# Kernel optimization log

Hardware: AMD Instinct MI355X
Metric: run time of the kernel (lower is better)

## Reference

```python
import jax, jax.numpy as jnp
import numpy as np

N = 8192
IN_DIM = 256
OUT_DIM = 64
ALPHA = 0.2  # LeakyReLU negative slope


def setup_inputs() -> dict:
    key = jax.random.key(0)
    k1, k2, k3 = jax.random.split(key, 3)
    h = jax.random.normal(k1, (N, IN_DIM), dtype=jnp.float32)
    adj = jnp.zeros((N, N), dtype=jnp.bool_)  # accepted by forward but unused (faithful to source)
    # xavier_uniform-ish scale for params
    W = jax.random.normal(k2, (IN_DIM, OUT_DIM), dtype=jnp.float32) * (1.414 * (2.0 / (IN_DIM + OUT_DIM)) ** 0.5)
    a = jax.random.normal(k3, (2 * OUT_DIM, 1), dtype=jnp.float32) * (1.414 * (2.0 / (2 * OUT_DIM + 1)) ** 0.5)
    return {"h": h, "adj": adj, "W": W, "a": a}


def reference(h, adj, W, a):
    # Wh: [N, D]
    Wh = h @ W
    d = Wh.shape[1]
    Wh1 = Wh @ a[:d]   # [N, 1]
    Wh2 = Wh @ a[d:]   # [N, 1]
    # e: [N, N] dense additive attention scores (adj is NOT used in the source)
    e = jax.nn.leaky_relu(Wh1 + Wh2.T, negative_slope=ALPHA)
    attention = jax.nn.softmax(e, axis=1)
    # dropout(p=0.6) is identity in eval mode
    h_prime = attention @ Wh  # [N, D]
    return jax.nn.elu(h_prime)
```

## Files before the change

kernel.cpp:

```cpp
#include <hip/hip_runtime.h>
#include <math.h>

#define NN 8192
#define KDIM 256
#define DD 64
#define NB 4096
#define NBLK 256
#define NTHR 512
#define RPB 32
#define CH 32
#define NCH 256
#define LRALPHA 0.2f

__device__ __forceinline__ unsigned f2k(float f) {
    unsigned u = __float_as_uint(f);
    return u ^ ((u >> 31) ? 0xFFFFFFFFu : 0x80000000u);
}
__device__ __forceinline__ float k2f(unsigned k) {
    return __uint_as_float((k & 0x80000000u) ? (k ^ 0x80000000u) : ~k);
}
__device__ __forceinline__ unsigned bucket_of(unsigned key, unsigned kmin, float scale) {
    unsigned d = key - kmin;
    unsigned b = (unsigned)((float)d * scale);
    return b > (NB - 1) ? (NB - 1) : b;
}

__device__ __forceinline__ void  cstf(float* p, float v) { __hip_atomic_store(p, v, __ATOMIC_RELAXED, __HIP_MEMORY_SCOPE_AGENT); }
__device__ __forceinline__ float cldf(const float* p)    { return __hip_atomic_load((float*)p, __ATOMIC_RELAXED, __HIP_MEMORY_SCOPE_AGENT); }
__device__ __forceinline__ unsigned cldu(const unsigned* p) { return __hip_atomic_load((unsigned*)p, __ATOMIC_RELAXED, __HIP_MEMORY_SCOPE_AGENT); }
__device__ __forceinline__ void cstu(unsigned* p, unsigned v) { __hip_atomic_store(p, v, __ATOMIC_RELAXED, __HIP_MEMORY_SCOPE_AGENT); }

__device__ __forceinline__ void gridbar(unsigned* flags, unsigned* rel, unsigned phase) {
    asm volatile("s_waitcnt vmcnt(0)" ::: "memory");
    __syncthreads();
    const int t = threadIdx.x;
    if (blockIdx.x == 0) {
        if (t == 0)
            cstu(&flags[0], phase);
        if (t < NBLK) {
            while (cldu(&flags[t]) < phase)
                __builtin_amdgcn_s_sleep(1);
        }
        __syncthreads();
        if (t == 0)
            cstu(rel, phase);
    } else {
        if (t == 0) {
            cstu(&flags[blockIdx.x], phase);
            while (cldu(rel) < phase)
                __builtin_amdgcn_s_sleep(1);
        }
        __syncthreads();
    }
}

__global__ __launch_bounds__(NTHR, 2) void k_fused(
    const float* __restrict__ h, const float* __restrict__ W,
    const float* __restrict__ a, float* __restrict__ out,
    float* Wh2g, float* sv, float* wnv, float* wpv, float* sg,
    float* cs_neg, float* cs_pos, float* cs_sn, float* cs_sp,
    float* PN, float* SP, float* PNs, float* SPs,
    int* cnt, unsigned* flags, unsigned* rel, unsigned* done)
{
    __shared__ int      ls_bstart[NB + 1];
    __shared__ float    ls_wh1[RPB];
    __shared__ float    ls_wh2[RPB];
    __shared__ unsigned ls_ra[8], ls_rb[8];
    __shared__ int      ls_wsum[8];
    __shared__ float    ls_cs[8][2 * DD];
    __shared__ float    ls_css[16];
    __shared__ float    ls_M2, ls_scale;
    __shared__ unsigned ls_kmin;

    const int t = threadIdx.x, bid = blockIdx.x;
    const int wv = t >> 6, lane = t & 63;
    const int rowBase = bid * RPB;

    float myrow[4];
    {
        const int r0 = rowBase + wv * 4;
        float acc0 = 0.f, acc1 = 0.f, acc2 = 0.f, acc3 = 0.f;
        #pragma unroll 2
        for (int k4 = 0; k4 < KDIM / 4; ++k4) {
            float w0 = W[(4 * k4 + 0) * DD + lane];
            float w1 = W[(4 * k4 + 1) * DD + lane];
            float w2 = W[(4 * k4 + 2) * DD + lane];
            float w3 = W[(4 * k4 + 3) * DD + lane];
            float4 h0 = *(const float4*)(h + (size_t)(r0 + 0) * KDIM + 4 * k4);
            float4 h1 = *(const float4*)(h + (size_t)(r0 + 1) * KDIM + 4 * k4);
            float4 h2 = *(const float4*)(h + (size_t)(r0 + 2) * KDIM + 4 * k4);
            float4 h3 = *(const float4*)(h + (size_t)(r0 + 3) * KDIM + 4 * k4);
            acc0 = fmaf(h0.x, w0, acc0); acc0 = fmaf(h0.y, w1, acc0);
            acc0 = fmaf(h0.z, w2, acc0); acc0 = fmaf(h0.w, w3, acc0);
            acc1 = fmaf(h1.x, w0, acc1); acc1 = fmaf(h1.y, w1, acc1);
            acc1 = fmaf(h1.z, w2, acc1); acc1 = fmaf(h1.w, w3, acc1);
            acc2 = fmaf(h2.x, w0, acc2); acc2 = fmaf(h2.y, w1, acc2);
            acc2 = fmaf(h2.z, w2, acc2); acc2 = fmaf(h2.w, w3, acc2);
            acc3 = fmaf(h3.x, w0, acc3); acc3 = fmaf(h3.y, w1, acc3);
            acc3 = fmaf(h3.z, w2, acc3); acc3 = fmaf(h3.w, w3, acc3);
        }
        myrow[0] = acc0; myrow[1] = acc1; myrow[2] = acc2; myrow[3] = acc3;
        float a1 = a[lane], a2 = a[DD + lane];
        #pragma unroll
        for (int i = 0; i < 4; ++i) {
            float r1 = myrow[i] * a1, r2 = myrow[i] * a2;
            #pragma unroll
            for (int off = 32; off > 0; off >>= 1) {
                r1 += __shfl_xor(r1, off, 64);
                r2 += __shfl_xor(r2, off, 64);
            }
            if (lane == 0) {
                cstf(&Wh2g[r0 + i], r2);
                ls_wh1[wv * 4 + i] = r1;
                ls_wh2[wv * 4 + i] = r2;
            }
        }
    }
    gridbar(flags, rel, 1);

    for (int i = t; i < NB; i += NTHR) ls_bstart[i] = 0;
    float v16[16];
    #pragma unroll
    for (int q = 0; q < 16; ++q)
        v16[q] = cldf(&Wh2g[t + q * NTHR]);
    {
        unsigned lmin = 0xFFFFFFFFu, lmax = 0u;
        #pragma unroll
        for (int q = 0; q < 16; ++q) {
            unsigned k = f2k(v16[q]);
            lmin = min(lmin, k); lmax = max(lmax, k);
        }
        #pragma unroll
        for (int off = 32; off > 0; off >>= 1) {
            lmin = min(lmin, (unsigned)__shfl_xor((int)lmin, off, 64));
            lmax = max(lmax, (unsigned)__shfl_xor((int)lmax, off, 64));
        }
        if (lane == 0) { ls_ra[wv] = lmin; ls_rb[wv] = lmax; }
    }
    __syncthreads();
    if (t == 0) {
        unsigned mn = ls_ra[0], mx = ls_rb[0];
        for (int i = 1; i < 8; ++i) { mn = min(mn, ls_ra[i]); mx = max(mx, ls_rb[i]); }
        ls_kmin = mn;
        ls_scale = (float)NB / ((float)(mx - mn) + 1.0f);
        ls_M2 = k2f(mx);
    }
    __syncthreads();
    const unsigned kmin = ls_kmin;
    const float scale = ls_scale;
    const float M2 = ls_M2;

    #pragma unroll
    for (int q = 0; q < 16; ++q)
        atomicAdd(&ls_bstart[bucket_of(f2k(v16[q]), kmin, scale)], 1);
    __syncthreads();
    {
        int s[8]; int tot = 0;
        #pragma unroll
        for (int j = 0; j < 8; ++j) { s[j] = ls_bstart[8 * t + j]; tot += s[j]; }
        int x = tot;
        #pragma unroll
        for (int off = 1; off < 64; off <<= 1) {
            int y = __shfl_up(x, off, 64);
            if (lane >= off) x += y;
        }
        if (lane == 63) ls_wsum[wv] = x;
        __syncthreads();
        int woff = 0;
        for (int w2 = 0; w2 < wv; ++w2) woff += ls_wsum[w2];
        int acc = woff + x - tot;
        #pragma unroll
        for (int j = 0; j < 8; ++j) { ls_bstart[8 * t + j] = acc; acc += s[j]; }
        if (t == 0) ls_bstart[NB] = NN;
    }
    __syncthreads();
    {
        int posl = 0;
        if (lane < 4) {
            unsigned b = bucket_of(f2k(ls_wh2[wv * 4 + lane]), kmin, scale);
            posl = ls_bstart[b] + atomicAdd(&cnt[b], 1);
        }
        #pragma unroll
        for (int i = 0; i < 4; ++i) {
            int lr = wv * 4 + i;
            float x = ls_wh2[lr];
            int pos = __shfl(posl, i, 64);
            cstf(&sg[(size_t)pos * DD + lane], myrow[i]);
            if (lane == 0) {
                cstf(&sv[pos], x);
                cstf(&wnv[pos], expf(LRALPHA * (x - M2)));
                cstf(&wpv[pos], expf(x - M2));
            }
        }
    }
    gridbar(flags, rel, 2);

    {
        int base = bid * CH + wv * 4;
        float g4[4], wn4[4], wp4[4];
        #pragma unroll
        for (int kk = 0; kk < 4; ++kk) {
            int k = base + kk;
            g4[kk]  = cldf(&sg[(size_t)k * DD + lane]);
            wn4[kk] = cldf(&wnv[k]);
            wp4[kk] = cldf(&wpv[k]);
        }
        float an = 0.f, ap = 0.f, sn = 0.f, sp = 0.f;
        #pragma unroll
        for (int kk = 0; kk < 4; ++kk) {
            an = fmaf(wn4[kk], g4[kk], an); ap = fmaf(wp4[kk], g4[kk], ap);
            sn += wn4[kk]; sp += wp4[kk];
        }
        ls_cs[wv][lane] = an; ls_cs[wv][DD + lane] = ap;
        if (lane == 0) { ls_css[wv] = sn; ls_css[8 + wv] = sp; }
        __syncthreads();
        if (wv == 0) {
            float s = 0.f;
            #pragma unroll
            for (int w2 = 0; w2 < 8; ++w2) s += ls_cs[w2][lane];
            cstf(&cs_neg[bid * DD + lane], s);
            if (lane == 0) { float ss = 0.f; for (int w2 = 0; w2 < 8; ++w2) ss += ls_css[w2]; cstf(&cs_sn[bid], ss); }
        } else if (wv == 1) {
            float s = 0.f;
            #pragma unroll
            for (int w2 = 0; w2 < 8; ++w2) s += ls_cs[w2][DD + lane];
            cstf(&cs_pos[bid * DD + lane], s);
            if (lane == 0) { float ss = 0.f; for (int w2 = 0; w2 < 8; ++w2) ss += ls_css[8 + w2]; cstf(&cs_sp[bid], ss); }
        }
    }
    asm volatile("s_waitcnt vmcnt(0)" ::: "memory");
    __syncthreads();
    if (t == 0)
        cstu(&flags[bid], 3u);

    if (bid == 0) {
        if (t < NBLK) { while (cldu(&flags[t]) < 3u) __builtin_amdgcn_s_sleep(1); }
        __syncthreads();
        const int c0 = wv * 32;
        float v[32];
        #pragma unroll
        for (int j = 0; j < 32; ++j) v[j] = cldf(&cs_neg[(c0 + j) * DD + lane]);
        float tot = 0.f;
        #pragma unroll
        for (int j = 0; j < 32; ++j) tot += v[j];
        ls_cs[wv][lane] = tot;
        __syncthreads();
        float acc = 0.f;
        for (int w2 = 0; w2 < wv; ++w2) acc += ls_cs[w2][lane];
        #pragma unroll
        for (int j = 0; j < 32; ++j) { cstf(&PN[(c0 + j) * DD + lane], acc); acc += v[j]; }
        if (wv == 7) cstf(&PN[NCH * DD + lane], acc);
        asm volatile("s_waitcnt vmcnt(0)" ::: "memory");
        __syncthreads();
        if (t == 0) cstu(&done[0], 1u);
    } else if (bid == 1) {
        if (t < NBLK) { while (cldu(&flags[t]) < 3u) __builtin_amdgcn_s_sleep(1); }
        __syncthreads();
        const int c0 = wv * 32;
        float v[32];
        #pragma unroll
        for (int j = 0; j < 32; ++j) v[j] = cldf(&cs_pos[(c0 + j) * DD + lane]);
        float tot = 0.f;
        #pragma unroll
        for (int j = 0; j < 32; ++j) tot += v[j];
        ls_cs[wv][lane] = tot;
        __syncthreads();
        float acc = 0.f;
        for (int w2 = wv + 1; w2 < 8; ++w2) acc += ls_cs[w2][lane];
        #pragma unroll
        for (int j = 31; j >= 0; --j) { acc += v[j]; cstf(&SP[(c0 + j) * DD + lane], acc); }
        if (wv == 7) cstf(&SP[NCH * DD + lane], 0.f);
        asm volatile("s_waitcnt vmcnt(0)" ::: "memory");
        __syncthreads();
        if (t == 0) cstu(&done[1], 1u);
    } else if (bid == 2) {
        if (t < NBLK) { while (cldu(&flags[t]) < 3u) __builtin_amdgcn_s_sleep(1); }
        __syncthreads();
        if (wv == 0) {
            float s[4];
            #pragma unroll
            for (int j = 0; j < 4; ++j) s[j] = cldf(&cs_sn[4 * lane + j]);
            float tot = s[0] + s[1] + s[2] + s[3];
            float x = tot;
            #pragma unroll
            for (int off = 1; off < 64; off <<= 1) {
                float y = __shfl_up(x, off, 64);
                if (lane >= off) x += y;
            }
            float acc = x - tot;
            #pragma unroll
            for (int j = 0; j < 4; ++j) { cstf(&PNs[4 * lane + j], acc); acc += s[j]; }
            if (lane == 63) cstf(&PNs[NCH], acc);
        } else if (wv == 1) {
            float s[4];
            #pragma unroll
            for (int j = 0; j < 4; ++j) s[j] = cldf(&cs_sp[4 * lane + j]);
            float tot = s[0] + s[1] + s[2] + s[3];
            float x = tot;
            #pragma unroll
            for (int off = 1; off < 64; off <<= 1) {
                float y = __shfl_down(x, off, 64);
                if (lane < 64 - off) x += y;
            }
            float acc = x - tot;
            #pragma unroll
            for (int j = 3; j >= 0; --j) { acc += s[j]; cstf(&SPs[4 * lane + j], acc); }
            if (lane == 63) cstf(&SPs[NCH], 0.f);
        }
        asm volatile("s_waitcnt vmcnt(0)" ::: "memory");
        __syncthreads();
        if (t == 0) cstu(&done[2], 1u);
    }

    int c0f4[4], c1e4[4];
    float cn4[4], dn4[4], cp4[4], dp4[4];
    #pragma unroll
    for (int i = 0; i < 4; ++i) {
        float tt = -ls_wh1[wv * 4 + i];
        unsigned kt = f2k(tt);
        int p0 = 0, p1 = 0;
        if (kt >= kmin) {
            unsigned b = bucket_of(kt, kmin, scale);
            p0 = ls_bstart[b]; p1 = ls_bstart[b + 1];
        }
        int c0f = p0 >> 5, c1e = (p1 + 31) >> 5;
        c0f4[i] = c0f; c1e4[i] = c1e;
        float nn_ = 0.f, dn_ = 0.f, np_ = 0.f, dp_ = 0.f;
        for (int base2 = c0f * CH; base2 < c1e * CH; base2 += 8) {
            float sv8[8], wn8[8], wp8[8], g8[8];
            #pragma unroll
            for (int jj = 0; jj < 8; ++jj) {
                int k = base2 + jj;
                sv8[jj] = cldf(&sv[k]);
                wn8[jj] = cldf(&wnv[k]);
                wp8[jj] = cldf(&wpv[k]);
                g8[jj]  = cldf(&sg[(size_t)k * DD + lane]);
            }
            #pragma unroll
            for (int jj = 0; jj < 8; ++jj) {
                if (sv8[jj] <= tt) { nn_ = fmaf(wn8[jj], g8[jj], nn_); dn_ += wn8[jj]; }
                else               { np_ = fmaf(wp8[jj], g8[jj], np_); dp_ += wp8[jj]; }
            }
        }
        cn4[i] = nn_; dn4[i] = dn_; cp4[i] = np_; dp4[i] = dp_;
    }

    if (t < 3) { while (cldu(&done[t]) < 1u) __builtin_amdgcn_s_sleep(1); }
    __syncthreads();

    float pn4[4], sp4[4], pns4[4], sps4[4];
    #pragma unroll
    for (int i = 0; i < 4; ++i) {
        pn4[i]  = cldf(&PN[c0f4[i] * DD + lane]);
        sp4[i]  = cldf(&SP[c1e4[i] * DD + lane]);
        pns4[i] = cldf(&PNs[c0f4[i]]);
        sps4[i] = cldf(&SPs[c1e4[i]]);
    }
    #pragma unroll
    for (int i = 0; i < 4; ++i) {
        int row = rowBase + wv * 4 + i;
        float w1 = ls_wh1[wv * 4 + i];
        float z = w1 + M2;
        float m = (z >= 0.f) ? z : LRALPHA * z;
        float c1 = expf(z - m);
        float c2 = expf(LRALPHA * z - m);
        float num = c2 * (pn4[i] + cn4[i]) + c1 * (sp4[i] + cp4[i]);
        float den = c2 * (pns4[i] + dn4[i]) + c1 * (sps4[i] + dp4[i]);
        float r = num / den;
        out[(size_t)row * DD + lane] = (r > 0.f) ? r : expm1f(r);
    }
}

extern "C" void kernel_launch(void* const* d_in, const int* in_sizes, int n_in,
                              void* d_out, int out_size, void* d_ws, size_t ws_size,
                              hipStream_t stream)
{
    const float* h = (const float*)d_in[0];
    const float* W = (const float*)d_in[2];
    const float* a = (const float*)d_in[3];
    float* out = (float*)d_out;
    float* ws = (float*)d_ws;

    float* Wh2g   = ws;
    float* sv     = Wh2g + NN;
    float* wnv    = sv + NN;
    float* wpv    = wnv + NN;
    float* sg     = wpv + NN;
    float* cs_neg = sg + (size_t)NN * DD;
    float* cs_pos = cs_neg + NCH * DD;
    float* cs_sn  = cs_pos + NCH * DD;
    float* cs_sp  = cs_sn + NCH;
    float* PN     = cs_sp + NCH;
    float* SP     = PN + (NCH + 1) * DD;
    float* PNs    = SP + (NCH + 1) * DD;
    float* SPs    = PNs + 320;
    unsigned* flags = (unsigned*)(SPs + 320);
    unsigned* rel   = flags + NBLK;
    unsigned* done  = rel + 64;
    int*   cnt    = (int*)(done + 64);

    hipMemsetAsync(flags, 0, (NBLK + 64 + 64 + NB) * sizeof(unsigned), stream);
    k_fused<<<NBLK, NTHR, 0, stream>>>(h, W, a, out,
        Wh2g, sv, wnv, wpv, sg,
        cs_neg, cs_pos, cs_sn, cs_sp,
        PN, SP, PNs, SPs,
        cnt, flags, rel, done);
}
```

Measured before the change: 89.70 us.

## Recompute exp weights on the fly and interleave boundary-chunk loops across rows

Drops the precomputed wnv/wpv weight arrays. The exp weights are now recomputed from sorted Wh2 values wherever they are needed, which cuts global stores and loads in exchange for extra exp instructions. The per-row boundary chunk scan is also restructured so all four rows of a wave load their 8-element batches together in one loop. This gives more memory-level parallelism, at the cost of higher register pressure and divergence from unequal trip counts.

```diff
diff --git a/kernel.cpp b/kernel.cpp
--- a/kernel.cpp
+++ b/kernel.cpp
@@ -57,7 +57,7 @@
 __global__ __launch_bounds__(NTHR, 2) void k_fused(
     const float* __restrict__ h, const float* __restrict__ W,
     const float* __restrict__ a, float* __restrict__ out,
-    float* Wh2g, float* sv, float* wnv, float* wpv, float* sg,
+    float* Wh2g, float* sv, float* sg,
     float* cs_neg, float* cs_pos, float* cs_sn, float* cs_sp,
     float* PN, float* SP, float* PNs, float* SPs,
     int* cnt, unsigned* flags, unsigned* rel, unsigned* done)
@@ -186,30 +186,27 @@
             float x = ls_wh2[lr];
             int pos = __shfl(posl, i, 64);
             cstf(&sg[(size_t)pos * DD + lane], myrow[i]);
-            if (lane == 0) {
-                cstf(&sv[pos], x);
-                cstf(&wnv[pos], expf(LRALPHA * (x - M2)));
-                cstf(&wpv[pos], expf(x - M2));
-            }
+            if (lane == 0) cstf(&sv[pos], x);
         }
     }
     gridbar(flags, rel, 2);
 
     {
         int base = bid * CH + wv * 4;
-        float g4[4], wn4[4], wp4[4];
+        float g4[4], sv4[4];
         #pragma unroll
         for (int kk = 0; kk < 4; ++kk) {
             int k = base + kk;
             g4[kk]  = cldf(&sg[(size_t)k * DD + lane]);
-            wn4[kk] = cldf(&wnv[k]);
-            wp4[kk] = cldf(&wpv[k]);
+            sv4[kk] = cldf(&sv[k]);
         }
         float an = 0.f, ap = 0.f, sn = 0.f, sp = 0.f;
         #pragma unroll
         for (int kk = 0; kk < 4; ++kk) {
-            an = fmaf(wn4[kk], g4[kk], an); ap = fmaf(wp4[kk], g4[kk], ap);
-            sn += wn4[kk]; sp += wp4[kk];
+            float wn = expf(LRALPHA * (sv4[kk] - M2));
+            float wp = expf(sv4[kk] - M2);
+            an = fmaf(wn, g4[kk], an); ap = fmaf(wp, g4[kk], ap);
+            sn += wn; sp += wp;
         }
         ls_cs[wv][lane] = an; ls_cs[wv][DD + lane] = ap;
         if (lane == 0) { ls_css[wv] = sn; ls_css[8 + wv] = sp; }
@@ -312,11 +309,13 @@
         if (t == 0) cstu(&done[2], 1u);
     }
 
-    int c0f4[4], c1e4[4];
-    float cn4[4], dn4[4], cp4[4], dp4[4];
+    int c0f4[4], c1e4[4], nb4[4];
+    float tt4[4];
+    int maxnb = 0;
     #pragma unroll
     for (int i = 0; i < 4; ++i) {
         float tt = -ls_wh1[wv * 4 + i];
+        tt4[i] = tt;
         unsigned kt = f2k(tt);
         int p0 = 0, p1 = 0;
         if (kt >= kmin) {
@@ -325,24 +324,40 @@
         }
         int c0f = p0 >> 5, c1e = (p1 + 31) >> 5;
         c0f4[i] = c0f; c1e4[i] = c1e;
-        float nn_ = 0.f, dn_ = 0.f, np_ = 0.f, dp_ = 0.f;
-        for (int base2 = c0f * CH; base2 < c1e * CH; base2 += 8) {
-            float sv8[8], wn8[8], wp8[8], g8[8];
-            #pragma unroll
-            for (int jj = 0; jj < 8; ++jj) {
-                int k = base2 + jj;
-                sv8[jj] = cldf(&sv[k]);
-                wn8[jj] = cldf(&wnv[k]);
-                wp8[jj] = cldf(&wpv[k]);
-                g8[jj]  = cldf(&sg[(size_t)k * DD + lane]);
-            }
-            #pragma unroll
-            for (int jj = 0; jj < 8; ++jj) {
-                if (sv8[jj] <= tt) { nn_ = fmaf(wn8[jj], g8[jj], nn_); dn_ += wn8[jj]; }
-                else               { np_ = fmaf(wp8[jj], g8[jj], np_); dp_ += wp8[jj]; }
-            }
-        }
-        cn4[i] = nn_; dn4[i] = dn_; cp4[i] = np_; dp4[i] = dp_;
+        nb4[i] = (c1e - c0f) * (CH / 8);
+        maxnb = max(maxnb, nb4[i]);
+    }
+    float cn4[4] = {0,0,0,0}, dn4[4] = {0,0,0,0}, cp4[4] = {0,0,0,0}, dp4[4] = {0,0,0,0};
+    for (int b = 0; b < maxnb; ++b) {
+        float sv8[4][8], g8[4][8];
+        #pragma unroll
+        for (int i = 0; i < 4; ++i) {
+            if (b < nb4[i]) {
+                int k0 = c0f4[i] * CH + b * 8;
+                #pragma unroll
+                for (int jj = 0; jj < 8; ++jj) {
+                    sv8[i][jj] = cldf(&sv[k0 + jj]);
+                    g8[i][jj]  = cldf(&sg[(size_t)(k0 + jj) * DD + lane]);
+                }
+            }
+        }
+        #pragma unroll
+        for (int i = 0; i < 4; ++i) {
+            if (b < nb4[i]) {
+                float tt = tt4[i];
+                #pragma unroll
+                for (int jj = 0; jj < 8; ++jj) {
+                    float svv = sv8[i][jj], g = g8[i][jj];
+                    if (svv <= tt) {
+                        float wn = expf(LRALPHA * (svv - M2));
+                        cn4[i] = fmaf(wn, g, cn4[i]); dn4[i] += wn;
+                    } else {
+                        float wp = expf(svv - M2);
+                        cp4[i] = fmaf(wp, g, cp4[i]); dp4[i] += wp;
+                    }
+                }
+            }
+        }
     }
 
     if (t < 3) { while (cldu(&done[t]) < 1u) __builtin_amdgcn_s_sleep(1); }
@@ -383,9 +398,7 @@
 
     float* Wh2g   = ws;
     float* sv     = Wh2g + NN;
-    float* wnv    = sv + NN;
-    float* wpv    = wnv + NN;
-    float* sg     = wpv + NN;
+    float* sg     = sv + NN;
     float* cs_neg = sg + (size_t)NN * DD;
     float* cs_pos = cs_neg + NCH * DD;
     float* cs_sn  = cs_pos + NCH * DD;
@@ -401,7 +414,7 @@
 
     hipMemsetAsync(flags, 0, (NBLK + 64 + 64 + NB) * sizeof(unsigned), stream);
     k_fused<<<NBLK, NTHR, 0, stream>>>(h, W, a, out,
-        Wh2g, sv, wnv, wpv, sg,
+        Wh2g, sv, sg,
         cs_neg, cs_pos, cs_sn, cs_sp,
         PN, SP, PNs, SPs,
         cnt, flags, rel, done);
```

Result: slower. 111.2 us (+24.0%).
